# Kernel tuning notes

Measured on AMD Instinct MI355X. Metric: run time of the kernel, lower is better.

The kernel has to match this reference:

```python
import jax, jax.numpy as jnp
import numpy as np

NUM_CLASSES = 10
LAMBDA_COORD = 5.0
LAMBDA_NOOBJ = 0.5
B, S, P = 2048, 26, 5 + NUM_CLASSES


def setup_inputs() -> dict:
    key = jax.random.key(0)
    k1, k2 = jax.random.split(key)
    predictions = jax.random.normal(k1, (B, S, S, P), dtype=jnp.float32)
    targets = jax.random.normal(k2, (B, S * S * P,), dtype=jnp.float32)
    return {"predictions": predictions, "targets": targets}


def reference(predictions, targets):
    b, s, _, p = predictions.shape
    pred = predictions.reshape(b, s * s, p)          # (B, S*S, 5+C)
    tgt = targets.reshape(b, s * s, -1)              # (B, S*S, 5+C)

    obj = tgt[..., 4] > 0                            # object mask per cell

    # Coordinate loss: lambda_coord * sum((pred_xywh - tgt_xywh)^2) over object cells
    coord_sq = jnp.sum((pred[..., :4] - tgt[..., :4]) ** 2, axis=-1)
    coord_loss = LAMBDA_COORD * jnp.sum(jnp.where(obj, coord_sq, 0.0))

    # Confidence loss: (sigmoid(p_conf) - t_conf)^2 on obj cells,
    # lambda_noobj * sigmoid(p_conf)^2 on no-obj cells (scalar MSE mean == squared diff)
    conf_p = jax.nn.sigmoid(pred[..., 4])
    conf_loss = jnp.sum(jnp.where(obj,
                                  (conf_p - tgt[..., 4]) ** 2,
                                  LAMBDA_NOOBJ * conf_p ** 2))

    # Classification loss: mean over C of squared diff per object cell, summed
    cls_sq = jnp.mean((pred[..., 5:5 + NUM_CLASSES] - tgt[..., 5:5 + NUM_CLASSES]) ** 2, axis=-1)
    class_loss = jnp.sum(jnp.where(obj, cls_sq, 0.0))

    total_loss = coord_loss + conf_loss + class_loss
    return (total_loss, coord_loss, conf_loss, class_loss)
```

## Files before the change

### kernel.cpp

```cpp
#include <hip/hip_runtime.h>

constexpr int   NUM_CLASSES  = 10;
constexpr float LAMBDA_COORD = 5.0f;
constexpr float LAMBDA_NOOBJ = 0.5f;
constexpr int   BLOCK = 256;
constexpr int   CELLS_PER_WAVE = 64;
constexpr int   F4_PER_WAVE    = 240;
constexpr int   NBINS = 256;

__global__ __launch_bounds__(BLOCK) void yolo_main(
    const float4* __restrict__ pred4,
    const float4* __restrict__ tgt4,
    float* __restrict__ ws)
{
    __shared__ float flag[4][CELLS_PER_WAVE + 1];

    const unsigned tid  = threadIdx.x;
    const unsigned wave = tid >> 6;
    const unsigned lane = tid & 63u;
    const bool     has3 = lane < 48u;

    const unsigned gw = blockIdx.x * 4u + wave;
    const unsigned fb = gw * F4_PER_WAVE;

    float4 t[4], p[4];
    t[0] = tgt4[fb + lane];
    t[1] = tgt4[fb + 64u + lane];
    t[2] = tgt4[fb + 128u + lane];
    t[3] = has3 ? tgt4[fb + 192u + lane] : float4{0.f, 0.f, 0.f, 0.f};
    p[0] = pred4[fb + lane];
    p[1] = pred4[fb + 64u + lane];
    p[2] = pred4[fb + 128u + lane];
    p[3] = has3 ? pred4[fb + 192u + lane] : float4{0.f, 0.f, 0.f, 0.f};

#pragma unroll
    for (int q = 0; q < 4; ++q) {
        unsigned lf4 = (q < 3) ? (lane + 64u * (unsigned)q) : (192u + lane);
        unsigned lb  = 4u * lf4;
        unsigned lcell = lb / 15u;
        unsigned j0    = lb - lcell * 15u;
        float tm[4] = {t[q].x, t[q].y, t[q].z, t[q].w};
#pragma unroll
        for (int m = 0; m < 4; ++m) {
            if (q == 3 && !has3) break;
            unsigned j   = j0 + (unsigned)m;
            bool     sec = j >= 15u;
            unsigned jj  = sec ? j - 15u : j;
            if (jj == 4u) flag[wave][lcell + (sec ? 1u : 0u)] = tm[m];
        }
    }

    float coord = 0.f, conf = 0.f, cls = 0.f;
#pragma unroll
    for (int q = 0; q < 4; ++q) {
        unsigned lf4 = (q < 3) ? (lane + 64u * (unsigned)q) : (192u + lane);
        unsigned lb  = 4u * lf4;
        unsigned lcell = lb / 15u;
        unsigned j0    = lb - lcell * 15u;
        float t4a = flag[wave][lcell];
        float t4b = flag[wave][lcell + 1u];
        float pm[4] = {p[q].x, p[q].y, p[q].z, p[q].w};
        float tm[4] = {t[q].x, t[q].y, t[q].z, t[q].w};

        float pc = 0.f, tc = 0.f;
        bool  hasc = false;

#pragma unroll
        for (int m = 0; m < 4; ++m) {
            if (q == 3 && !has3) break;
            unsigned j   = j0 + (unsigned)m;
            bool     sec = j >= 15u;
            unsigned jj  = sec ? j - 15u : j;
            float    t4  = sec ? t4b : t4a;
            bool     obj = t4 > 0.f;

            float d  = pm[m] - tm[m];
            float sq = d * d;

            if (jj == 4u) { pc = pm[m]; tc = tm[m]; hasc = true; }
            else if (obj) {
                if (jj < 4u) coord += sq;
                else         cls   += sq;
            }
        }
        if (hasc) {
            float e   = __expf(-pc);
            float sig = __builtin_amdgcn_rcpf(1.f + e);
            float ds  = sig - tc;
            conf += (tc > 0.f) ? ds * ds : LAMBDA_NOOBJ * sig * sig;
        }
    }

#pragma unroll
    for (int off = 32; off > 0; off >>= 1) {
        coord += __shfl_down(coord, off);
        conf  += __shfl_down(conf,  off);
        cls   += __shfl_down(cls,   off);
    }

    __shared__ float s[3][4];
    if (lane == 0) { s[0][wave] = coord; s[1][wave] = conf; s[2][wave] = cls; }
    __syncthreads();

    if (tid == 0) {
        unsigned bin = (blockIdx.x & (NBINS - 1u)) * 3u;
        atomicAdd(&ws[bin + 0], s[0][0] + s[0][1] + s[0][2] + s[0][3]);
        atomicAdd(&ws[bin + 1], s[1][0] + s[1][1] + s[1][2] + s[1][3]);
        atomicAdd(&ws[bin + 2], s[2][0] + s[2][1] + s[2][2] + s[2][3]);
    }
}

__global__ __launch_bounds__(BLOCK) void yolo_finalize(
    const float* __restrict__ ws, float* __restrict__ out)
{
    float c0 = 0.f, c1 = 0.f, c2 = 0.f;
    for (unsigned i = threadIdx.x; i < (unsigned)NBINS; i += BLOCK) {
        c0 += ws[3u * i + 0];
        c1 += ws[3u * i + 1];
        c2 += ws[3u * i + 2];
    }
#pragma unroll
    for (int off = 32; off > 0; off >>= 1) {
        c0 += __shfl_down(c0, off);
        c1 += __shfl_down(c1, off);
        c2 += __shfl_down(c2, off);
    }
    __shared__ float s[3][4];
    int wave = threadIdx.x >> 6, lane = threadIdx.x & 63;
    if (lane == 0) { s[0][wave] = c0; s[1][wave] = c1; s[2][wave] = c2; }
    __syncthreads();
    if (threadIdx.x == 0) {
        float coord = LAMBDA_COORD * (s[0][0] + s[0][1] + s[0][2] + s[0][3]);
        float conf  =                 s[1][0] + s[1][1] + s[1][2] + s[1][3];
        float cls   = (1.f / NUM_CLASSES) * (s[2][0] + s[2][1] + s[2][2] + s[2][3]);
        out[0] = coord + conf + cls;
        out[1] = coord;
        out[2] = conf;
        out[3] = cls;
    }
}

extern "C" void kernel_launch(void* const* d_in, const int* in_sizes, int n_in,
                              void* d_out, int out_size, void* d_ws, size_t ws_size,
                              hipStream_t stream) {
    const float* pred = (const float*)d_in[0];
    const float* tgt  = (const float*)d_in[1];
    float* out = (float*)d_out;
    float* ws  = (float*)d_ws;

    unsigned total  = (unsigned)in_sizes[0];
    unsigned ncells = total / 15u;
    unsigned nwaves = ncells / CELLS_PER_WAVE;
    unsigned nblk   = nwaves / 4u;

    hipMemsetAsync(ws, 0, NBINS * 3 * sizeof(float), stream);
    yolo_main<<<nblk, BLOCK, 0, stream>>>((const float4*)pred, (const float4*)tgt, ws);
    yolo_finalize<<<1, BLOCK, 0, stream>>>(ws, out);
}
```

Before: 183.5 us.

## Use persistent grid-stride waves with double-buffered tile prefetch

The kernel now launches a fixed grid of 1024 blocks, and each wave loops over several 64-cell tiles with a grid stride instead of handling one tile. It alternates two register tile buffers so that the global loads for the next tile are issued before the current tile is computed, hiding memory latency. The per-lane cell and offset index math is hoisted out of the loop, and fewer blocks means fewer atomic adds into the bins. The cost is higher register pressure from holding two tiles, which may lower occupancy.

```diff
diff --git a/kernel.cpp b/kernel.cpp
--- a/kernel.cpp
+++ b/kernel.cpp
@@ -4,71 +4,57 @@
 constexpr float LAMBDA_COORD = 5.0f;
 constexpr float LAMBDA_NOOBJ = 0.5f;
 constexpr int   BLOCK = 256;
-constexpr int   CELLS_PER_WAVE = 64;
-constexpr int   F4_PER_WAVE    = 240;
+constexpr int   F4_PER_TILE = 240;
+constexpr int   NBLK  = 1024;
 constexpr int   NBINS = 256;
 
-__global__ __launch_bounds__(BLOCK) void yolo_main(
-    const float4* __restrict__ pred4,
-    const float4* __restrict__ tgt4,
-    float* __restrict__ ws)
+struct Tile { float4 t[4], p[4]; };
+
+__device__ __forceinline__ void load_tile(
+    const float4* __restrict__ pred4, const float4* __restrict__ tgt4,
+    unsigned tile, unsigned lane, bool has3, Tile& T)
 {
-    __shared__ float flag[4][CELLS_PER_WAVE + 1];
+    unsigned fb = tile * (unsigned)F4_PER_TILE;
+    T.t[0] = tgt4[fb + lane];
+    T.t[1] = tgt4[fb + 64u + lane];
+    T.t[2] = tgt4[fb + 128u + lane];
+    T.t[3] = has3 ? tgt4[fb + 192u + lane] : float4{0.f, 0.f, 0.f, 0.f};
+    T.p[0] = pred4[fb + lane];
+    T.p[1] = pred4[fb + 64u + lane];
+    T.p[2] = pred4[fb + 128u + lane];
+    T.p[3] = has3 ? pred4[fb + 192u + lane] : float4{0.f, 0.f, 0.f, 0.f};
+}
 
-    const unsigned tid  = threadIdx.x;
-    const unsigned wave = tid >> 6;
-    const unsigned lane = tid & 63u;
-    const bool     has3 = lane < 48u;
-
-    const unsigned gw = blockIdx.x * 4u + wave;
-    const unsigned fb = gw * F4_PER_WAVE;
-
-    float4 t[4], p[4];
-    t[0] = tgt4[fb + lane];
-    t[1] = tgt4[fb + 64u + lane];
-    t[2] = tgt4[fb + 128u + lane];
-    t[3] = has3 ? tgt4[fb + 192u + lane] : float4{0.f, 0.f, 0.f, 0.f};
-    p[0] = pred4[fb + lane];
-    p[1] = pred4[fb + 64u + lane];
-    p[2] = pred4[fb + 128u + lane];
-    p[3] = has3 ? pred4[fb + 192u + lane] : float4{0.f, 0.f, 0.f, 0.f};
-
+__device__ __forceinline__ void compute_tile(
+    const Tile& T, float* __restrict__ flagrow,
+    const unsigned* __restrict__ lcellq, const unsigned* __restrict__ j0q,
+    bool has3, float& coord, float& conf, float& cls)
+{
 #pragma unroll
     for (int q = 0; q < 4; ++q) {
-        unsigned lf4 = (q < 3) ? (lane + 64u * (unsigned)q) : (192u + lane);
-        unsigned lb  = 4u * lf4;
-        unsigned lcell = lb / 15u;
-        unsigned j0    = lb - lcell * 15u;
-        float tm[4] = {t[q].x, t[q].y, t[q].z, t[q].w};
+        float tm[4] = {T.t[q].x, T.t[q].y, T.t[q].z, T.t[q].w};
 #pragma unroll
         for (int m = 0; m < 4; ++m) {
             if (q == 3 && !has3) break;
-            unsigned j   = j0 + (unsigned)m;
+            unsigned j   = j0q[q] + (unsigned)m;
             bool     sec = j >= 15u;
             unsigned jj  = sec ? j - 15u : j;
-            if (jj == 4u) flag[wave][lcell + (sec ? 1u : 0u)] = tm[m];
+            if (jj == 4u) flagrow[lcellq[q] + (sec ? 1u : 0u)] = tm[m];
         }
     }
-
-    float coord = 0.f, conf = 0.f, cls = 0.f;
 #pragma unroll
     for (int q = 0; q < 4; ++q) {
-        unsigned lf4 = (q < 3) ? (lane + 64u * (unsigned)q) : (192u + lane);
-        unsigned lb  = 4u * lf4;
-        unsigned lcell = lb / 15u;
-        unsigned j0    = lb - lcell * 15u;
-        float t4a = flag[wave][lcell];
-        float t4b = flag[wave][lcell + 1u];
-        float pm[4] = {p[q].x, p[q].y, p[q].z, p[q].w};
-        float tm[4] = {t[q].x, t[q].y, t[q].z, t[q].w};
+        float t4a = flagrow[lcellq[q]];
+        float t4b = flagrow[lcellq[q] + 1u];
+        float pm[4] = {T.p[q].x, T.p[q].y, T.p[q].z, T.p[q].w};
+        float tm[4] = {T.t[q].x, T.t[q].y, T.t[q].z, T.t[q].w};
 
         float pc = 0.f, tc = 0.f;
         bool  hasc = false;
-
 #pragma unroll
         for (int m = 0; m < 4; ++m) {
             if (q == 3 && !has3) break;
-            unsigned j   = j0 + (unsigned)m;
+            unsigned j   = j0q[q] + (unsigned)m;
             bool     sec = j >= 15u;
             unsigned jj  = sec ? j - 15u : j;
             float    t4  = sec ? t4b : t4a;
@@ -88,6 +74,55 @@
             float sig = __builtin_amdgcn_rcpf(1.f + e);
             float ds  = sig - tc;
             conf += (tc > 0.f) ? ds * ds : LAMBDA_NOOBJ * sig * sig;
+        }
+    }
+}
+
+__global__ __launch_bounds__(BLOCK) void yolo_main(
+    const float4* __restrict__ pred4,
+    const float4* __restrict__ tgt4,
+    float* __restrict__ ws,
+    unsigned ntiles)
+{
+    __shared__ float flag[4][65];
+
+    const unsigned tid  = threadIdx.x;
+    const unsigned wave = tid >> 6;
+    const unsigned lane = tid & 63u;
+    const bool     has3 = lane < 48u;
+    float* flagrow = flag[wave];
+
+    unsigned lcellq[4], j0q[4];
+#pragma unroll
+    for (int q = 0; q < 4; ++q) {
+        unsigned lf4 = (q < 3) ? (lane + 64u * (unsigned)q) : (192u + lane);
+        unsigned lb  = 4u * lf4;
+        lcellq[q] = lb / 15u;
+        j0q[q]    = lb - 15u * lcellq[q];
+    }
+
+    const unsigned gw = blockIdx.x * 4u + wave;
+    const unsigned nw = gridDim.x * 4u;
+
+    float coord = 0.f, conf = 0.f, cls = 0.f;
+
+    Tile A, B;
+    unsigned tile = gw;
+    if (tile < ntiles) {
+        load_tile(pred4, tgt4, tile, lane, has3, A);
+        for (;;) {
+            unsigned t1 = tile + nw;
+            bool v1 = t1 < ntiles;
+            if (v1) load_tile(pred4, tgt4, t1, lane, has3, B);
+            compute_tile(A, flagrow, lcellq, j0q, has3, coord, conf, cls);
+            if (!v1) break;
+
+            unsigned t2 = t1 + nw;
+            bool v2 = t2 < ntiles;
+            if (v2) load_tile(pred4, tgt4, t2, lane, has3, A);
+            compute_tile(B, flagrow, lcellq, j0q, has3, coord, conf, cls);
+            if (!v2) break;
+            tile = t2;
         }
     }
 
@@ -150,10 +185,10 @@
 
     unsigned total  = (unsigned)in_sizes[0];
     unsigned ncells = total / 15u;
-    unsigned nwaves = ncells / CELLS_PER_WAVE;
-    unsigned nblk   = nwaves / 4u;
+    unsigned ntiles = ncells / 64u;
 
     hipMemsetAsync(ws, 0, NBINS * 3 * sizeof(float), stream);
-    yolo_main<<<nblk, BLOCK, 0, stream>>>((const float4*)pred, (const float4*)tgt, ws);
+    yolo_main<<<NBLK, BLOCK, 0, stream>>>(
+        (const float4*)pred, (const float4*)tgt, ws, ntiles);
     yolo_finalize<<<1, BLOCK, 0, stream>>>(ws, out);
 }
```

After: 185.8 us. No clear change (+1.2%).

## Process four tiles per wave and replace atomics with per-block partial writes

Applied to the files above, without the earlier changes.

Each wave now loads and processes four 64-cell tiles instead of one, issuing all loads up front so more memory requests are in flight per wave, and the grid shrinks fourfold to a hardcoded 1352 blocks. The per-block partial sums are written to distinct workspace slots instead of atomically added into bins, which removes the hipMemsetAsync launch and the atomics. The conf-element handling is rewritten with precomputed offsets and branchless selects. In exchange, register pressure rises (32 float4 values per lane), occupancy may drop, and the block count is tied to the fixed input size.

```diff
diff --git a/kernel.cpp b/kernel.cpp
--- a/kernel.cpp
+++ b/kernel.cpp
@@ -4,16 +4,16 @@
 constexpr float LAMBDA_COORD = 5.0f;
 constexpr float LAMBDA_NOOBJ = 0.5f;
 constexpr int   BLOCK = 256;
-constexpr int   CELLS_PER_WAVE = 64;
-constexpr int   F4_PER_WAVE    = 240;
-constexpr int   NBINS = 256;
+constexpr int   F4_PER_TILE   = 240;
+constexpr int   TILES_PER_WAVE = 4;
+constexpr int   NBLK = 1352;
 
 __global__ __launch_bounds__(BLOCK) void yolo_main(
     const float4* __restrict__ pred4,
     const float4* __restrict__ tgt4,
     float* __restrict__ ws)
 {
-    __shared__ float flag[4][CELLS_PER_WAVE + 1];
+    __shared__ float flag[4][TILES_PER_WAVE][66];
 
     const unsigned tid  = threadIdx.x;
     const unsigned wave = tid >> 6;
@@ -21,73 +21,83 @@
     const bool     has3 = lane < 48u;
 
     const unsigned gw = blockIdx.x * 4u + wave;
-    const unsigned fb = gw * F4_PER_WAVE;
+    const unsigned t0 = gw * (unsigned)TILES_PER_WAVE;
 
-    float4 t[4], p[4];
-    t[0] = tgt4[fb + lane];
-    t[1] = tgt4[fb + 64u + lane];
-    t[2] = tgt4[fb + 128u + lane];
-    t[3] = has3 ? tgt4[fb + 192u + lane] : float4{0.f, 0.f, 0.f, 0.f};
-    p[0] = pred4[fb + lane];
-    p[1] = pred4[fb + 64u + lane];
-    p[2] = pred4[fb + 128u + lane];
-    p[3] = has3 ? pred4[fb + 192u + lane] : float4{0.f, 0.f, 0.f, 0.f};
+    float4 T[TILES_PER_WAVE][4], P[TILES_PER_WAVE][4];
+#pragma unroll
+    for (int r = 0; r < TILES_PER_WAVE; ++r) {
+        unsigned fb = (t0 + (unsigned)r) * (unsigned)F4_PER_TILE;
+        T[r][0] = tgt4[fb + lane];
+        T[r][1] = tgt4[fb + 64u + lane];
+        T[r][2] = tgt4[fb + 128u + lane];
+        T[r][3] = has3 ? tgt4[fb + 192u + lane] : float4{0.f, 0.f, 0.f, 0.f};
+    }
+#pragma unroll
+    for (int r = 0; r < TILES_PER_WAVE; ++r) {
+        unsigned fb = (t0 + (unsigned)r) * (unsigned)F4_PER_TILE;
+        P[r][0] = pred4[fb + lane];
+        P[r][1] = pred4[fb + 64u + lane];
+        P[r][2] = pred4[fb + 128u + lane];
+        P[r][3] = has3 ? pred4[fb + 192u + lane] : float4{0.f, 0.f, 0.f, 0.f};
+    }
 
+    unsigned lcellq[4], j0q[4];
 #pragma unroll
     for (int q = 0; q < 4; ++q) {
         unsigned lf4 = (q < 3) ? (lane + 64u * (unsigned)q) : (192u + lane);
         unsigned lb  = 4u * lf4;
-        unsigned lcell = lb / 15u;
-        unsigned j0    = lb - lcell * 15u;
-        float tm[4] = {t[q].x, t[q].y, t[q].z, t[q].w};
+        lcellq[q] = lb / 15u;
+        j0q[q]    = lb - 15u * lcellq[q];
+    }
+
 #pragma unroll
-        for (int m = 0; m < 4; ++m) {
+    for (int r = 0; r < TILES_PER_WAVE; ++r) {
+#pragma unroll
+        for (int q = 0; q < 4; ++q) {
             if (q == 3 && !has3) break;
-            unsigned j   = j0 + (unsigned)m;
-            bool     sec = j >= 15u;
-            unsigned jj  = sec ? j - 15u : j;
-            if (jj == 4u) flag[wave][lcell + (sec ? 1u : 0u)] = tm[m];
+            unsigned j0 = j0q[q];
+            if (j0 >= 1u && j0 <= 4u) {
+                float tm[4] = {T[r][q].x, T[r][q].y, T[r][q].z, T[r][q].w};
+                unsigned m = 4u - j0;
+                float v = (m == 0u) ? tm[0] : (m == 1u) ? tm[1] : (m == 2u) ? tm[2] : tm[3];
+                flag[wave][r][lcellq[q]] = v;
+            }
         }
     }
 
     float coord = 0.f, conf = 0.f, cls = 0.f;
 #pragma unroll
-    for (int q = 0; q < 4; ++q) {
-        unsigned lf4 = (q < 3) ? (lane + 64u * (unsigned)q) : (192u + lane);
-        unsigned lb  = 4u * lf4;
-        unsigned lcell = lb / 15u;
-        unsigned j0    = lb - lcell * 15u;
-        float t4a = flag[wave][lcell];
-        float t4b = flag[wave][lcell + 1u];
-        float pm[4] = {p[q].x, p[q].y, p[q].z, p[q].w};
-        float tm[4] = {t[q].x, t[q].y, t[q].z, t[q].w};
-
-        float pc = 0.f, tc = 0.f;
-        bool  hasc = false;
+    for (int r = 0; r < TILES_PER_WAVE; ++r) {
+#pragma unroll
+        for (int q = 0; q < 4; ++q) {
+            if (q == 3 && !has3) break;
+            unsigned j0 = j0q[q], lcell = lcellq[q];
+            float t4a = flag[wave][r][lcell];
+            float t4b = flag[wave][r][lcell + 1u];
+            float pm[4] = {P[r][q].x, P[r][q].y, P[r][q].z, P[r][q].w};
+            float tm[4] = {T[r][q].x, T[r][q].y, T[r][q].z, T[r][q].w};
 
 #pragma unroll
-        for (int m = 0; m < 4; ++m) {
-            if (q == 3 && !has3) break;
-            unsigned j   = j0 + (unsigned)m;
-            bool     sec = j >= 15u;
-            unsigned jj  = sec ? j - 15u : j;
-            float    t4  = sec ? t4b : t4a;
-            bool     obj = t4 > 0.f;
-
-            float d  = pm[m] - tm[m];
-            float sq = d * d;
-
-            if (jj == 4u) { pc = pm[m]; tc = tm[m]; hasc = true; }
-            else if (obj) {
-                if (jj < 4u) coord += sq;
-                else         cls   += sq;
+            for (int m = 0; m < 4; ++m) {
+                unsigned j   = j0 + (unsigned)m;
+                bool     sec = j >= 15u;
+                unsigned jj  = sec ? j - 15u : j;
+                float    t4  = sec ? t4b : t4a;
+                bool     obj = t4 > 0.f;
+                float d  = pm[m] - tm[m];
+                float sq = d * d;
+                coord += (obj && jj < 4u) ? sq : 0.f;
+                cls   += (obj && jj > 4u) ? sq : 0.f;
             }
-        }
-        if (hasc) {
-            float e   = __expf(-pc);
-            float sig = __builtin_amdgcn_rcpf(1.f + e);
-            float ds  = sig - tc;
-            conf += (tc > 0.f) ? ds * ds : LAMBDA_NOOBJ * sig * sig;
+            if (j0 >= 1u && j0 <= 4u) {
+                unsigned m = 4u - j0;
+                float pc = (m == 0u) ? pm[0] : (m == 1u) ? pm[1] : (m == 2u) ? pm[2] : pm[3];
+                float tc = (m == 0u) ? tm[0] : (m == 1u) ? tm[1] : (m == 2u) ? tm[2] : tm[3];
+                float e   = __expf(-pc);
+                float sig = __builtin_amdgcn_rcpf(1.f + e);
+                float ds  = sig - tc;
+                conf += (tc > 0.f) ? ds * ds : LAMBDA_NOOBJ * sig * sig;
+            }
         }
     }
 
@@ -103,10 +113,9 @@
     __syncthreads();
 
     if (tid == 0) {
-        unsigned bin = (blockIdx.x & (NBINS - 1u)) * 3u;
-        atomicAdd(&ws[bin + 0], s[0][0] + s[0][1] + s[0][2] + s[0][3]);
-        atomicAdd(&ws[bin + 1], s[1][0] + s[1][1] + s[1][2] + s[1][3]);
-        atomicAdd(&ws[bin + 2], s[2][0] + s[2][1] + s[2][2] + s[2][3]);
+        ws[blockIdx.x]                = s[0][0] + s[0][1] + s[0][2] + s[0][3];
+        ws[NBLK + blockIdx.x]         = s[1][0] + s[1][1] + s[1][2] + s[1][3];
+        ws[2 * NBLK + blockIdx.x]     = s[2][0] + s[2][1] + s[2][2] + s[2][3];
     }
 }
 
@@ -114,10 +123,10 @@
     const float* __restrict__ ws, float* __restrict__ out)
 {
     float c0 = 0.f, c1 = 0.f, c2 = 0.f;
-    for (unsigned i = threadIdx.x; i < (unsigned)NBINS; i += BLOCK) {
-        c0 += ws[3u * i + 0];
-        c1 += ws[3u * i + 1];
-        c2 += ws[3u * i + 2];
+    for (unsigned i = threadIdx.x; i < (unsigned)NBLK; i += BLOCK) {
+        c0 += ws[i];
+        c1 += ws[NBLK + i];
+        c2 += ws[2 * NBLK + i];
     }
 #pragma unroll
     for (int off = 32; off > 0; off >>= 1) {
@@ -148,12 +157,6 @@
     float* out = (float*)d_out;
     float* ws  = (float*)d_ws;
 
-    unsigned total  = (unsigned)in_sizes[0];
-    unsigned ncells = total / 15u;
-    unsigned nwaves = ncells / CELLS_PER_WAVE;
-    unsigned nblk   = nwaves / 4u;
-
-    hipMemsetAsync(ws, 0, NBINS * 3 * sizeof(float), stream);
-    yolo_main<<<nblk, BLOCK, 0, stream>>>((const float4*)pred, (const float4*)tgt, ws);
+    yolo_main<<<NBLK, BLOCK, 0, stream>>>((const float4*)pred, (const float4*)tgt, ws);
     yolo_finalize<<<1, BLOCK, 0, stream>>>(ws, out);
 }
```

New measurement: 184.7 us. No clear change (+0.7%).
